# Performance work log

Measured on AMD Instinct MI355X. Metric: run time of the kernel, lower is better.

The kernel has to match this reference:

```python
import jax, jax.numpy as jnp
import numpy as np

# ---- model / data constants ----
B, N, D, L = 32, 96, 64, 5          # graphs, nodes per graph, hidden, layers
EP = 768                             # directed edges per graph (symmetrized in to_dense)
NODE_VOCAB = 11                      # matches LocalFWL2(..., 11, 5, 'instance')
EDGE_VOCAB = 5                       # edge labels 0..4; index 5 = 'no edge' embedding row
EPS = 1e-5


def setup_inputs() -> dict:
    key = jax.random.key(0)
    ks = jax.random.split(key, 12)
    # block-contiguous batch: graph b owns nodes [b*N, (b+1)*N)
    x = jax.random.randint(ks[0], (B * N,), 0, NODE_VOCAB)
    u = jax.random.randint(ks[1], (B, EP), 0, N)
    v = jax.random.randint(ks[2], (B, EP), 0, N)
    off = (jnp.arange(B) * N)[:, None]
    edge_index = jnp.stack([(u + off).reshape(-1), (v + off).reshape(-1)], axis=0)
    edge_attr = jax.random.randint(ks[3], (B * EP,), 0, EDGE_VOCAB)
    s = 0.1
    inv = 1.0 / np.sqrt(D)
    return {
        "x": x,
        "edge_index": edge_index,
        "edge_attr": edge_attr,
        "node_emb": jax.random.normal(ks[4], (NODE_VOCAB, D), jnp.float32) * s,
        "edge_emb": jax.random.normal(ks[5], (EDGE_VOCAB + 1, D), jnp.float32) * s,
        "W1": jax.random.normal(ks[6], (L, D, D), jnp.float32) * inv,
        "b1": jnp.zeros((L, D), jnp.float32),
        "W2": jax.random.normal(ks[7], (L, D, D), jnp.float32) * inv,
        "b2": jnp.zeros((L, D), jnp.float32),
        "Wm": jax.random.normal(ks[8], (L, D, D), jnp.float32) * inv,
        "bm": jnp.zeros((L, D), jnp.float32),
        "gamma": jnp.ones((L, D), jnp.float32),
        "beta": jnp.zeros((L, D), jnp.float32),
        "pool_w": jax.random.normal(ks[9], (D, 1), jnp.float32) * inv,
        "pool_b": jnp.zeros((1,), jnp.float32),
    }


def reference(x, edge_index, edge_attr, node_emb, edge_emb,
              W1, b1, W2, b2, Wm, bm, gamma, beta, pool_w, pool_b):
    # ---- to_dense: sparse edge list -> dense per-graph edge-label matrix ----
    g = edge_index[0] // N
    u = edge_index[0] % N
    v = edge_index[1] % N
    A = jnp.full((B, N, N), EDGE_VOCAB, dtype=jnp.int32)        # EDGE_VOCAB = no-edge
    ea = edge_attr.astype(jnp.int32)
    A = A.at[g, u, v].set(ea)
    A = A.at[g, v, u].set(ea)                                    # undirected
    adj = (A != EDGE_VOCAB).astype(node_emb.dtype)               # [B,N,N]

    # ---- pair-state init: W_uv = h_u + h_v + edge_emb(A_uv) ----
    H = node_emb[x.reshape(B, N)]                                # [B,N,D]
    W = H[:, :, None, :] + H[:, None, :, :] + edge_emb[A]        # [B,N,N,D]

    # ---- local FWL(2) layers ----
    for l in range(L):
        h1 = jax.nn.relu(jnp.einsum('buwd,de->buwe', W, W1[l]) + b1[l])
        h2 = jax.nn.relu(jnp.einsum('bwvd,de->bwve', W, W2[l]) + b2[l])
        # aggregate over w restricted to neighbors of v (local FWL2)
        M = jnp.einsum('buwd,bwv,bwvd->buvd', h1, adj, h2)       # [B,N,N,D]
        W = W + jnp.einsum('buvd,de->buve', M, Wm[l]) + bm[l]
        # instance norm over the pair dims (u,v), per graph, per channel
        mu = W.mean(axis=(1, 2), keepdims=True)
        var = W.var(axis=(1, 2), keepdims=True)
        W = gamma[l] * (W - mu) * jax.lax.rsqrt(var + EPS) + beta[l]
        W = jax.nn.relu(W)

    # ---- pooling: sum over all pairs, then Linear(D, 1), squeeze ----
    pooled = W.sum(axis=(1, 2))                                  # [B,D]
    return (pooled @ pool_w + pool_b).squeeze(-1)                # [B]
```

## Files before the change

### kernel.cpp

```cpp
#include <hip/hip_runtime.h>
#include <hip/hip_bf16.h>

#define B_ 32
#define N_ 96
#define D_ 64
#define L_ 5
#define BE_ 24576
#define NN_ 9216
#define BNN_ 294912
#define EPS_ 1e-5f
#define INV_NN (1.0f/9216.0f)

typedef unsigned short u16;
typedef unsigned int u32;
typedef __attribute__((ext_vector_type(8))) short bf16x8;
typedef __attribute__((ext_vector_type(4))) float f32x4;

__device__ __forceinline__ float bf2f(u16 r){ return __uint_as_float(((u32)r) << 16); }
__device__ __forceinline__ u32 f2bf(float f){
  u32 u = __float_as_uint(f);
  return (u + 0x7fffu + ((u >> 16) & 1u)) >> 16;
}
__device__ __forceinline__ u32 pack2(float lo, float hi){
  return f2bf(lo) | (f2bf(hi) << 16);
}

__global__ void k_scatter(const int* __restrict__ ei, const int* __restrict__ ea,
                          int* __restrict__ A)
{
  int e = blockIdx.x * 256 + threadIdx.x;
  if (e >= BE_) return;
  int a = ei[e], bnode = ei[BE_ + e];
  int g = a / N_;
  int u = a % N_;
  int v = bnode % N_;
  int lab = ea[e] & 7;
  int base = g * NN_;
  atomicMax(&A[base + u * N_ + v], ((e + 1) << 3) | lab);
  atomicMax(&A[base + v * N_ + u], ((BE_ + e + 1) << 3) | lab);
}

__launch_bounds__(256)
__global__ void k_winit(const int* __restrict__ x, const int* __restrict__ A,
                        const float* __restrict__ nemb, const float* __restrict__ eemb,
                        u16* __restrict__ W)
{
  int gid = blockIdx.x * 256 + threadIdx.x;
  int d = (gid & 15) * 4;
  int p = gid >> 4;
  int b = p / NN_;
  int rem = p % NN_;
  int u = rem / N_;
  int v = rem % N_;
  int xu = x[b * N_ + u], xv = x[b * N_ + v];
  int pk = A[p];
  int lab = pk ? (pk & 7) : 5;
  float4 nu = *(const float4*)(nemb + xu * 64 + d);
  float4 nv = *(const float4*)(nemb + xv * 64 + d);
  float4 ee = *(const float4*)(eemb + lab * 64 + d);
  uint2 o;
  o.x = pack2(nu.x + nv.x + ee.x, nu.y + nv.y + ee.y);
  o.y = pack2(nu.z + nv.z + ee.z, nu.w + nv.w + ee.w);
  ((uint2*)W)[gid] = o;
}

__global__ void k_prep(const float* __restrict__ W1, const float* __restrict__ W2,
                       const float* __restrict__ Wm, u16* __restrict__ WT)
{
  int idx = blockIdx.x * 256 + threadIdx.x;
  if (idx >= 15 * 4096) return;
  int l3 = idx >> 12;
  int r  = idx & 4095;
  int e = r >> 6, d = r & 63;
  int l = l3 / 3, which = l3 % 3;
  const float* s = which == 0 ? W1 : which == 1 ? W2 : Wm;
  WT[idx] = (u16)f2bf(s[l * 4096 + d * 64 + e]);
}

__launch_bounds__(256, 4)
__global__ void k_lin2(const u16* __restrict__ W, const u16* __restrict__ WT1,
                       const u16* __restrict__ WT2,
                       const float* __restrict__ b1l, const float* __restrict__ b2l,
                       const int* __restrict__ A,
                       const float* __restrict__ pst, const float* __restrict__ gml,
                       const float* __restrict__ btl, float* __restrict__ nsF,
                       int use_norm, u16* __restrict__ h1, u16* __restrict__ g2)
{
  __shared__ u16 Cs[64 * 264];
  __shared__ float nsS[128];
  const int tid = threadIdx.x;
  const int wave = tid >> 6, lane = tid & 63;
  const int lm = lane & 15, lg = lane >> 4;
  const int b = blockIdx.x / 36;
  const int qbase = (blockIdx.x % 36) * 256;

  if (use_norm) {
    if (tid < 128) {
      const float* p = pst + ((size_t)b * 144) * 128 + tid;
      float a0 = 0.f, a1 = 0.f, a2 = 0.f, a3 = 0.f;
      for (int i = 0; i < 144; i += 4) {
        a0 += p[(size_t)i * 128];
        a1 += p[(size_t)(i + 1) * 128];
        a2 += p[(size_t)(i + 2) * 128];
        a3 += p[(size_t)(i + 3) * 128];
      }
      nsS[tid] = (a0 + a1) + (a2 + a3);
    }
    __syncthreads();
  }

  float sc[2][8], sh[2][8];
  if (use_norm) {
    #pragma unroll
    for (int s = 0; s < 2; ++s) {
      int d0 = s * 32 + lg * 8;
      #pragma unroll
      for (int j = 0; j < 8; ++j) {
        int d = d0 + j;
        float S1 = nsS[d], S2 = nsS[64 + d];
        float mu = S1 * INV_NN;
        float var = fmaf(S2, INV_NN, -mu * mu);
        float s0 = gml[d] * rsqrtf(var + EPS_);
        sc[s][j] = s0;
        sh[s][j] = fmaf(-mu, s0, btl[d]);
      }
    }
    if ((blockIdx.x % 36) == 0 && tid < 64) {
      float S1 = nsS[tid], S2 = nsS[64 + tid];
      float mu = S1 * INV_NN;
      float var = fmaf(S2, INV_NN, -mu * mu);
      float s0 = gml[tid] * rsqrtf(var + EPS_);
      nsF[((size_t)b * 64 + tid) * 2]     = s0;
      nsF[((size_t)b * 64 + tid) * 2 + 1] = fmaf(-mu, s0, btl[tid]);
    }
  } else {
    #pragma unroll
    for (int s = 0; s < 2; ++s)
      #pragma unroll
      for (int j = 0; j < 8; ++j) { sc[s][j] = 1.f; sh[s][j] = 0.f; }
  }

  bf16x8 bF[4][2];
  int flags[4];
  #pragma unroll
  for (int qt = 0; qt < 4; ++qt) {
    int q = qbase + wave * 64 + qt * 16 + lm;
    const u16* wrow = W + ((size_t)b * NN_ + q) * 64;
    flags[qt] = A[b * NN_ + q];
    #pragma unroll
    for (int s = 0; s < 2; ++s) {
      bf16x8 raw = *(const bf16x8*)(wrow + s * 32 + lg * 8);
      if (use_norm) {
        bf16x8 bb;
        #pragma unroll
        for (int j = 0; j < 8; ++j) {
          float v = bf2f((u16)raw[j]);
          v = fmaxf(fmaf(v, sc[s][j], sh[s][j]), 0.f);
          bb[j] = (short)f2bf(v);
        }
        bF[qt][s] = bb;
      } else {
        bF[qt][s] = raw;
      }
    }
  }

  const f32x4 zf = {0.f, 0.f, 0.f, 0.f};

  {
    bf16x8 aF[4][2];
    #pragma unroll
    for (int et = 0; et < 4; ++et)
      #pragma unroll
      for (int s = 0; s < 2; ++s)
        aF[et][s] = *(const bf16x8*)(WT1 + (et * 16 + lm) * 64 + s * 32 + lg * 8);
    float4 bsv[4];
    #pragma unroll
    for (int et = 0; et < 4; ++et) bsv[et] = *(const float4*)(b1l + et * 16 + lg * 4);
    #pragma unroll
    for (int qt = 0; qt < 4; ++qt) {
      f32x4 acc[4] = {zf, zf, zf, zf};
      #pragma unroll
      for (int s = 0; s < 2; ++s)
        #pragma unroll
        for (int et = 0; et < 4; ++et)
          acc[et] = __builtin_amdgcn_mfma_f32_16x16x32_bf16(aF[et][s], bF[qt][s], acc[et], 0, 0, 0);
      int col = wave * 64 + qt * 16 + lm;
      #pragma unroll
      for (int et = 0; et < 4; ++et) {
        float bv[4] = {bsv[et].x, bsv[et].y, bsv[et].z, bsv[et].w};
        #pragma unroll
        for (int r = 0; r < 4; ++r)
          Cs[(et * 16 + lg * 4 + r) * 264 + col] = (u16)f2bf(fmaxf(acc[et][r] + bv[r], 0.f));
      }
    }
  }
  __syncthreads();
  {
    u16* ob = h1 + (size_t)b * 64 * NN_ + qbase;
    for (int i = tid; i < 2048; i += 256) {
      int e = i >> 5, qc = (i & 31) * 8;
      uint4 val = *(const uint4*)&Cs[e * 264 + qc];
      *(uint4*)(ob + (size_t)e * NN_ + qc) = val;
    }
  }
  __syncthreads();

  {
    bf16x8 aF[4][2];
    #pragma unroll
    for (int et = 0; et < 4; ++et)
      #pragma unroll
      for (int s = 0; s < 2; ++s)
        aF[et][s] = *(const bf16x8*)(WT2 + (et * 16 + lm) * 64 + s * 32 + lg * 8);
    float4 bsv[4];
    #pragma unroll
    for (int et = 0; et < 4; ++et) bsv[et] = *(const float4*)(b2l + et * 16 + lg * 4);
    #pragma unroll
    for (int qt = 0; qt < 4; ++qt) {
      f32x4 acc[4] = {zf, zf, zf, zf};
      #pragma unroll
      for (int s = 0; s < 2; ++s)
        #pragma unroll
        for (int et = 0; et < 4; ++et)
          acc[et] = __builtin_amdgcn_mfma_f32_16x16x32_bf16(aF[et][s], bF[qt][s], acc[et], 0, 0, 0);
      int col = wave * 64 + qt * 16 + lm;
      #pragma unroll
      for (int et = 0; et < 4; ++et) {
        float bv[4] = {bsv[et].x, bsv[et].y, bsv[et].z, bsv[et].w};
        #pragma unroll
        for (int r = 0; r < 4; ++r) {
          float v = fmaxf(acc[et][r] + bv[r], 0.f);
          if (!flags[qt]) v = 0.f;
          Cs[(et * 16 + lg * 4 + r) * 264 + col] = (u16)f2bf(v);
        }
      }
    }
  }
  __syncthreads();
  {
    u16* ob = g2 + (size_t)b * 64 * NN_ + qbase;
    for (int i = tid; i < 2048; i += 256) {
      int e = i >> 5, qc = (i & 31) * 8;
      uint4 val = *(const uint4*)&Cs[e * 264 + qc];
      *(uint4*)(ob + (size_t)e * NN_ + qc) = val;
    }
  }
}

__launch_bounds__(256, 4)
__global__ void k_einsum(const u16* __restrict__ h1, const u16* __restrict__ g2n,
                         u16* __restrict__ M)
{
  __shared__ u32 Bt[96 * 60];
  u16* Cst = (u16*)Bt;
  const int tid = threadIdx.x;
  const int wave = tid >> 6, lane = tid & 63;
  const int lm = lane & 15, lg = lane >> 4;
  const int bd = blockIdx.x;
  const u16* h1p = h1 + (size_t)bd * NN_;
  const u16* g2p = g2n + (size_t)bd * NN_;
  const int u0 = (wave & 1) * 48, v0 = (wave >> 1) * 48;

  #pragma unroll
  for (int it = 0; it < 9; ++it) {
    int p = it * 256 + tid;
    int wp = p / 48, vh = (p % 48) * 2;
    u32 a = *(const u32*)(g2p + (2 * wp) * 96 + vh);
    u32 c = *(const u32*)(g2p + (2 * wp + 1) * 96 + vh);
    Bt[vh * 60 + wp]       = (a & 0xffffu) | (c << 16);
    Bt[(vh + 1) * 60 + wp] = (a >> 16) | (c & 0xffff0000u);
  }

  bf16x8 aF[3][3];
  #pragma unroll
  for (int t = 0; t < 3; ++t)
    #pragma unroll
    for (int s = 0; s < 3; ++s)
      aF[t][s] = *(const bf16x8*)(h1p + (u0 + t * 16 + lm) * 96 + s * 32 + lg * 8);
  __syncthreads();

  const f32x4 zf = {0.f, 0.f, 0.f, 0.f};
  f32x4 acc[3][3];
  #pragma unroll
  for (int i = 0; i < 3; ++i)
    #pragma unroll
    for (int j = 0; j < 3; ++j) acc[i][j] = zf;

  #pragma unroll
  for (int s = 0; s < 3; ++s) {
    bf16x8 bb[3];
    #pragma unroll
    for (int vt = 0; vt < 3; ++vt)
      bb[vt] = *(const bf16x8*)&Bt[(v0 + vt * 16 + lm) * 60 + s * 16 + lg * 4];
    #pragma unroll
    for (int ut = 0; ut < 3; ++ut)
      #pragma unroll
      for (int vt = 0; vt < 3; ++vt)
        acc[ut][vt] = __builtin_amdgcn_mfma_f32_16x16x32_bf16(aF[ut][s], bb[vt], acc[ut][vt], 0, 0, 0);
  }
  __syncthreads();

  #pragma unroll
  for (int ut = 0; ut < 3; ++ut)
    #pragma unroll
    for (int vt = 0; vt < 3; ++vt)
      #pragma unroll
      for (int r = 0; r < 4; ++r)
        Cst[(u0 + ut * 16 + lg * 4 + r) * 104 + v0 + vt * 16 + lm] = (u16)f2bf(acc[ut][vt][r]);
  __syncthreads();
  u16* Mp = M + (size_t)bd * NN_;
  for (int i = tid; i < 1152; i += 256) {
    int u = i / 12, vc = (i % 12) * 8;
    uint4 val = *(const uint4*)&Cst[u * 104 + vc];
    *(uint4*)(Mp + u * 96 + vc) = val;
  }
}

__launch_bounds__(128)
__global__ void k_update(const u16* __restrict__ M, const u16* __restrict__ WmT,
                         const float* __restrict__ bml, u16* __restrict__ W,
                         const float* __restrict__ nsF, int use_norm,
                         float* __restrict__ pst)
{
  __shared__ u16 Mt[64 * 64];
  __shared__ float red[2][128];
  const int tid = threadIdx.x;
  const int wave = tid >> 6, lane = tid & 63;
  const int lm = lane & 15, lg = lane >> 4;
  const int b = blockIdx.x / 144;
  const int qi = blockIdx.x % 144;
  const int qblk = qi * 64;

  bf16x8 aF[4][2];
  #pragma unroll
  for (int et = 0; et < 4; ++et)
    #pragma unroll
    for (int s = 0; s < 2; ++s)
      aF[et][s] = *(const bf16x8*)(WmT + (et * 16 + lm) * 64 + s * 32 + lg * 8);

  uint2 wres[2][4];
  #pragma unroll
  for (int qtL = 0; qtL < 2; ++qtL) {
    int qg = qblk + (wave * 2 + qtL) * 16 + lm;
    const u16* Wp = W + ((size_t)b * NN_ + qg) * 64;
    #pragma unroll
    for (int et = 0; et < 4; ++et)
      wres[qtL][et] = *(const uint2*)(Wp + et * 16 + lg * 4);
  }

  float scn[4][4], shn[4][4];
  if (use_norm) {
    #pragma unroll
    for (int et = 0; et < 4; ++et) {
      int e0 = et * 16 + lg * 4;
      float4 t0 = *(const float4*)(nsF + ((size_t)b * 64 + e0) * 2);
      float4 t1 = *(const float4*)(nsF + ((size_t)b * 64 + e0) * 2 + 4);
      scn[et][0] = t0.x; shn[et][0] = t0.y; scn[et][1] = t0.z; shn[et][1] = t0.w;
      scn[et][2] = t1.x; shn[et][2] = t1.y; scn[et][3] = t1.z; shn[et][3] = t1.w;
    }
  } else {
    #pragma unroll
    for (int et = 0; et < 4; ++et)
      #pragma unroll
      for (int r = 0; r < 4; ++r) { scn[et][r] = 1.f; shn[et][r] = 0.f; }
  }

  {
    const int dpl = tid >> 1;
    const int qob = tid & 1;
    const u16* Mb = M + (size_t)(b * 64 + dpl) * NN_ + qblk;
    #pragma unroll
    for (int t = 0; t < 4; ++t) {
      int qo = qob + t * 2;
      uint4 v = *(const uint4*)(Mb + qo * 8);
      u32 ws[4] = {v.x, v.y, v.z, v.w};
      #pragma unroll
      for (int h = 0; h < 4; ++h) {
        int j0 = h * 2;
        int q0 = qo * 8 + j0;
        int slot0 = (dpl >> 3) ^ j0 ^ (qo & 7);
        int slot1 = (dpl >> 3) ^ (j0 + 1) ^ (qo & 7);
        Mt[q0 * 64 + slot0 * 8 + (dpl & 7)]       = (u16)(ws[h] & 0xffffu);
        Mt[(q0 + 1) * 64 + slot1 * 8 + (dpl & 7)] = (u16)(ws[h] >> 16);
      }
    }
  }
  __syncthreads();

  const f32x4 zf = {0.f, 0.f, 0.f, 0.f};
  f32x4 acc[2][4];
  #pragma unroll
  for (int i = 0; i < 2; ++i)
    #pragma unroll
    for (int j = 0; j < 4; ++j) acc[i][j] = zf;

  #pragma unroll
  for (int qtL = 0; qtL < 2; ++qtL) {
    int ql = (wave * 2 + qtL) * 16 + lm;
    bf16x8 bF[2];
    #pragma unroll
    for (int s = 0; s < 2; ++s) {
      int slot = (s * 4 + lg) ^ (ql & 7) ^ ((ql >> 3) & 7);
      bF[s] = *(const bf16x8*)&Mt[ql * 64 + slot * 8];
    }
    #pragma unroll
    for (int s = 0; s < 2; ++s)
      #pragma unroll
      for (int et = 0; et < 4; ++et)
        acc[qtL][et] = __builtin_amdgcn_mfma_f32_16x16x32_bf16(aF[et][s], bF[s], acc[qtL][et], 0, 0, 0);
  }

  float s1[4][4], s2[4][4];
  #pragma unroll
  for (int i = 0; i < 4; ++i)
    #pragma unroll
    for (int j = 0; j < 4; ++j) { s1[i][j] = 0.f; s2[i][j] = 0.f; }

  #pragma unroll
  for (int et = 0; et < 4; ++et) {
    int e0 = et * 16 + lg * 4;
    float4 bs = *(const float4*)(bml + e0);
    float bv[4] = {bs.x, bs.y, bs.z, bs.w};
    #pragma unroll
    for (int qtL = 0; qtL < 2; ++qtL) {
      int qg = qblk + (wave * 2 + qtL) * 16 + lm;
      u16* Wp = W + ((size_t)b * NN_ + qg) * 64 + e0;
      uint2 wo = wres[qtL][et];
      float wv[4] = {bf2f((u16)(wo.x & 0xffff)), bf2f((u16)(wo.x >> 16)),
                     bf2f((u16)(wo.y & 0xffff)), bf2f((u16)(wo.y >> 16))};
      float o[4];
      #pragma unroll
      for (int r = 0; r < 4; ++r) {
        float res = use_norm ? fmaxf(fmaf(wv[r], scn[et][r], shn[et][r]), 0.f) : wv[r];
        float val = acc[qtL][et][r] + bv[r] + res;
        o[r] = val;
        s1[et][r] += val;
        s2[et][r] = fmaf(val, val, s2[et][r]);
      }
      uint2 ov;
      ov.x = pack2(o[0], o[1]);
      ov.y = pack2(o[2], o[3]);
      *(uint2*)Wp = ov;
    }
  }

  #pragma unroll
  for (int et = 0; et < 4; ++et)
    #pragma unroll
    for (int r = 0; r < 4; ++r) {
      float a = s1[et][r], c = s2[et][r];
      a += __shfl_xor(a, 1, 64); a += __shfl_xor(a, 2, 64);
      a += __shfl_xor(a, 4, 64); a += __shfl_xor(a, 8, 64);
      c += __shfl_xor(c, 1, 64); c += __shfl_xor(c, 2, 64);
      c += __shfl_xor(c, 4, 64); c += __shfl_xor(c, 8, 64);
      if (lm == 0) {
        int e = et * 16 + lg * 4 + r;
        red[wave][e]      = a;
        red[wave][64 + e] = c;
      }
    }
  __syncthreads();
  if (tid < 128)
    pst[((size_t)b * 144 + qi) * 128 + tid] = red[0][tid] + red[1][tid];
}

__launch_bounds__(256)
__global__ void k_pool(const u16* __restrict__ W,
                       const float* __restrict__ pst,
                       const float* __restrict__ gml, const float* __restrict__ btl,
                       const float* __restrict__ pw, const float* __restrict__ pb,
                       float* __restrict__ out)
{
  __shared__ float nsS[128];
  const int b = blockIdx.x / 24;
  const int chunk = blockIdx.x % 24;
  const int tid = threadIdx.x;
  if (tid < 128) {
    const float* p = pst + ((size_t)b * 144) * 128 + tid;
    float a0 = 0.f, a1 = 0.f, a2 = 0.f, a3 = 0.f;
    for (int i = 0; i < 144; i += 4) {
      a0 += p[(size_t)i * 128];
      a1 += p[(size_t)(i + 1) * 128];
      a2 += p[(size_t)(i + 2) * 128];
      a3 += p[(size_t)(i + 3) * 128];
    }
    nsS[tid] = (a0 + a1) + (a2 + a3);
  }
  __syncthreads();
  const int e = tid & 63;
  float S1 = nsS[e], S2 = nsS[64 + e];
  float mu = S1 * INV_NN;
  float var = fmaf(S2, INV_NN, -mu * mu);
  float rsig = rsqrtf(var + EPS_);
  float scl = gml[e] * rsig;
  float shf = fmaf(-mu, scl, btl[e]);
  float pwv = pw[e];
  const u16* base = W + (size_t)b * NN_ * 64 + chunk * 24576;
  float s = 0.f;
  for (int k = 0; k < 96; k++) {
    float w = bf2f(base[k * 256 + tid]);
    s += fmaxf(fmaf(w, scl, shf), 0.f) * pwv;
  }
  for (int o = 32; o; o >>= 1) s += __shfl_down(s, o, 64);
  __shared__ float rs[4];
  if ((tid & 63) == 0) rs[tid >> 6] = s;
  __syncthreads();
  if (tid == 0) {
    float t = rs[0] + rs[1] + rs[2] + rs[3];
    if (chunk == 0) t += pb[0];
    atomicAdd(&out[b], t);
  }
}

extern "C" void kernel_launch(void* const* d_in, const int* in_sizes, int n_in,
                              void* d_out, int out_size, void* d_ws, size_t ws_size,
                              hipStream_t stream) {
  const int*   x    = (const int*)d_in[0];
  const int*   ei   = (const int*)d_in[1];
  const int*   ea   = (const int*)d_in[2];
  const float* nemb = (const float*)d_in[3];
  const float* eemb = (const float*)d_in[4];
  const float* W1   = (const float*)d_in[5];
  const float* b1   = (const float*)d_in[6];
  const float* W2   = (const float*)d_in[7];
  const float* b2   = (const float*)d_in[8];
  const float* Wm   = (const float*)d_in[9];
  const float* bm   = (const float*)d_in[10];
  const float* gm   = (const float*)d_in[11];
  const float* bt   = (const float*)d_in[12];
  const float* pw   = (const float*)d_in[13];
  const float* pb   = (const float*)d_in[14];

  char* ws = (char*)d_ws;
  const size_t OFF_A  = 0;
  const size_t OFF_W  = 1179648;
  const size_t OFF_H1 = 38928384;
  const size_t OFF_G2 = 76677120;
  const size_t OFF_M  = 114425856;
  const size_t OFF_PS = 152174592;
  const size_t OFF_NF = 154533888;
  const size_t OFF_WT = 154550272;
  const size_t NEED   = OFF_WT + 122880;
  if (ws_size < NEED) return;

  int*   A     = (int*)(ws + OFF_A);
  u16*   W     = (u16*)(ws + OFF_W);
  u16*   h1    = (u16*)(ws + OFF_H1);
  u16*   g2n   = (u16*)(ws + OFF_G2);
  u16*   M     = (u16*)(ws + OFF_M);
  float* pst   = (float*)(ws + OFF_PS);
  float* nsF   = (float*)(ws + OFF_NF);
  u16*   WT    = (u16*)(ws + OFF_WT);
  float* out   = (float*)d_out;

  hipMemsetAsync(A, 0, 1179648, stream);
  hipMemsetAsync(out, 0, 32 * sizeof(float), stream);

  k_prep<<<240, 256, 0, stream>>>(W1, W2, Wm, WT);
  k_scatter<<<96, 256, 0, stream>>>(ei, ea, A);
  k_winit<<<18432, 256, 0, stream>>>(x, A, nemb, eemb, W);

  for (int l = 0; l < L_; l++) {
    int un = (l > 0);
    const float* gml = un ? gm + (l - 1) * 64 : gm;
    const float* btl = un ? bt + (l - 1) * 64 : bt;
    k_lin2<<<1152, 256, 0, stream>>>(W, WT + (l * 3 + 0) * 4096, WT + (l * 3 + 1) * 4096,
                                     b1 + l * 64, b2 + l * 64, A, pst, gml, btl, nsF,
                                     un, h1, g2n);
    k_einsum<<<2048, 256, 0, stream>>>(h1, g2n, M);
    k_update<<<4608, 128, 0, stream>>>(M, WT + (l * 3 + 2) * 4096, bm + l * 64, W,
                                       nsF, un, pst);
  }
  k_pool<<<768, 256, 0, stream>>>(W, pst, gm + 4 * 64, bt + 4 * 64, pw, pb, out);
}
```

Baseline: 551.0 us.

## Hoist instance-norm stats into separate kernel and halve k_lin2 tile

Moves the per-graph instance-norm reduction (summing 144 partial stat rows) out of every k_lin2 and k_pool block into a small k_ns kernel that writes scale/shift once per graph. k_lin2 then just loads precomputed scale/shift. Its tile is halved to 128 pairs per block with smaller shared memory, doubling the grid and raising the occupancy hint to 8. This removes redundant reduction work done by every block, at the cost of extra kernel launches per layer.

```diff
diff --git a/kernel.cpp b/kernel.cpp
--- a/kernel.cpp
+++ b/kernel.cpp
@@ -77,37 +77,46 @@
   WT[idx] = (u16)f2bf(s[l * 4096 + d * 64 + e]);
 }
 
-__launch_bounds__(256, 4)
+__launch_bounds__(128)
+__global__ void k_ns(const float* __restrict__ pst, const float* __restrict__ gml,
+                     const float* __restrict__ btl, float* __restrict__ nsF)
+{
+  __shared__ float nsS[128];
+  const int b = blockIdx.x;
+  const int tid = threadIdx.x;
+  const float* p = pst + ((size_t)b * 144) * 128 + tid;
+  float a0 = 0.f, a1 = 0.f, a2 = 0.f, a3 = 0.f;
+  for (int i = 0; i < 144; i += 4) {
+    a0 += p[(size_t)i * 128];
+    a1 += p[(size_t)(i + 1) * 128];
+    a2 += p[(size_t)(i + 2) * 128];
+    a3 += p[(size_t)(i + 3) * 128];
+  }
+  nsS[tid] = (a0 + a1) + (a2 + a3);
+  __syncthreads();
+  if (tid < 64) {
+    float S1 = nsS[tid], S2 = nsS[64 + tid];
+    float mu = S1 * INV_NN;
+    float var = fmaf(S2, INV_NN, -mu * mu);
+    float s0 = gml[tid] * rsqrtf(var + EPS_);
+    nsF[((size_t)b * 64 + tid) * 2]     = s0;
+    nsF[((size_t)b * 64 + tid) * 2 + 1] = fmaf(-mu, s0, btl[tid]);
+  }
+}
+
+__launch_bounds__(256, 8)
 __global__ void k_lin2(const u16* __restrict__ W, const u16* __restrict__ WT1,
                        const u16* __restrict__ WT2,
                        const float* __restrict__ b1l, const float* __restrict__ b2l,
-                       const int* __restrict__ A,
-                       const float* __restrict__ pst, const float* __restrict__ gml,
-                       const float* __restrict__ btl, float* __restrict__ nsF,
+                       const int* __restrict__ A, const float* __restrict__ nsF,
                        int use_norm, u16* __restrict__ h1, u16* __restrict__ g2)
 {
-  __shared__ u16 Cs[64 * 264];
-  __shared__ float nsS[128];
+  __shared__ u16 Cs[64 * 136];
   const int tid = threadIdx.x;
   const int wave = tid >> 6, lane = tid & 63;
   const int lm = lane & 15, lg = lane >> 4;
-  const int b = blockIdx.x / 36;
-  const int qbase = (blockIdx.x % 36) * 256;
-
-  if (use_norm) {
-    if (tid < 128) {
-      const float* p = pst + ((size_t)b * 144) * 128 + tid;
-      float a0 = 0.f, a1 = 0.f, a2 = 0.f, a3 = 0.f;
-      for (int i = 0; i < 144; i += 4) {
-        a0 += p[(size_t)i * 128];
-        a1 += p[(size_t)(i + 1) * 128];
-        a2 += p[(size_t)(i + 2) * 128];
-        a3 += p[(size_t)(i + 3) * 128];
-      }
-      nsS[tid] = (a0 + a1) + (a2 + a3);
-    }
-    __syncthreads();
-  }
+  const int b = blockIdx.x / 72;
+  const int qbase = (blockIdx.x % 72) * 128;
 
   float sc[2][8], sh[2][8];
   if (use_norm) {
@@ -115,23 +124,10 @@
     for (int s = 0; s < 2; ++s) {
       int d0 = s * 32 + lg * 8;
       #pragma unroll
-      for (int j = 0; j < 8; ++j) {
-        int d = d0 + j;
-        float S1 = nsS[d], S2 = nsS[64 + d];
-        float mu = S1 * INV_NN;
-        float var = fmaf(S2, INV_NN, -mu * mu);
-        float s0 = gml[d] * rsqrtf(var + EPS_);
-        sc[s][j] = s0;
-        sh[s][j] = fmaf(-mu, s0, btl[d]);
-      }
-    }
-    if ((blockIdx.x % 36) == 0 && tid < 64) {
-      float S1 = nsS[tid], S2 = nsS[64 + tid];
-      float mu = S1 * INV_NN;
-      float var = fmaf(S2, INV_NN, -mu * mu);
-      float s0 = gml[tid] * rsqrtf(var + EPS_);
-      nsF[((size_t)b * 64 + tid) * 2]     = s0;
-      nsF[((size_t)b * 64 + tid) * 2 + 1] = fmaf(-mu, s0, btl[tid]);
+      for (int j = 0; j < 8; j += 2) {
+        float4 t = *(const float4*)(nsF + ((size_t)b * 64 + d0 + j) * 2);
+        sc[s][j] = t.x; sh[s][j] = t.y; sc[s][j + 1] = t.z; sh[s][j + 1] = t.w;
+      }
     }
   } else {
     #pragma unroll
@@ -140,11 +136,11 @@
       for (int j = 0; j < 8; ++j) { sc[s][j] = 1.f; sh[s][j] = 0.f; }
   }
 
-  bf16x8 bF[4][2];
-  int flags[4];
-  #pragma unroll
-  for (int qt = 0; qt < 4; ++qt) {
-    int q = qbase + wave * 64 + qt * 16 + lm;
+  bf16x8 bF[2][2];
+  int flags[2];
+  #pragma unroll
+  for (int qt = 0; qt < 2; ++qt) {
+    int q = qbase + wave * 32 + qt * 16 + lm;
     const u16* wrow = W + ((size_t)b * NN_ + q) * 64;
     flags[qt] = A[b * NN_ + q];
     #pragma unroll
@@ -178,29 +174,29 @@
     #pragma unroll
     for (int et = 0; et < 4; ++et) bsv[et] = *(const float4*)(b1l + et * 16 + lg * 4);
     #pragma unroll
-    for (int qt = 0; qt < 4; ++qt) {
+    for (int qt = 0; qt < 2; ++qt) {
       f32x4 acc[4] = {zf, zf, zf, zf};
       #pragma unroll
       for (int s = 0; s < 2; ++s)
         #pragma unroll
         for (int et = 0; et < 4; ++et)
           acc[et] = __builtin_amdgcn_mfma_f32_16x16x32_bf16(aF[et][s], bF[qt][s], acc[et], 0, 0, 0);
-      int col = wave * 64 + qt * 16 + lm;
+      int col = wave * 32 + qt * 16 + lm;
       #pragma unroll
       for (int et = 0; et < 4; ++et) {
         float bv[4] = {bsv[et].x, bsv[et].y, bsv[et].z, bsv[et].w};
         #pragma unroll
         for (int r = 0; r < 4; ++r)
-          Cs[(et * 16 + lg * 4 + r) * 264 + col] = (u16)f2bf(fmaxf(acc[et][r] + bv[r], 0.f));
+          Cs[(et * 16 + lg * 4 + r) * 136 + col] = (u16)f2bf(fmaxf(acc[et][r] + bv[r], 0.f));
       }
     }
   }
   __syncthreads();
   {
     u16* ob = h1 + (size_t)b * 64 * NN_ + qbase;
-    for (int i = tid; i < 2048; i += 256) {
-      int e = i >> 5, qc = (i & 31) * 8;
-      uint4 val = *(const uint4*)&Cs[e * 264 + qc];
+    for (int i = tid; i < 1024; i += 256) {
+      int e = i >> 4, qc = (i & 15) * 8;
+      uint4 val = *(const uint4*)&Cs[e * 136 + qc];
       *(uint4*)(ob + (size_t)e * NN_ + qc) = val;
     }
   }
@@ -217,14 +213,14 @@
     #pragma unroll
     for (int et = 0; et < 4; ++et) bsv[et] = *(const float4*)(b2l + et * 16 + lg * 4);
     #pragma unroll
-    for (int qt = 0; qt < 4; ++qt) {
+    for (int qt = 0; qt < 2; ++qt) {
       f32x4 acc[4] = {zf, zf, zf, zf};
       #pragma unroll
       for (int s = 0; s < 2; ++s)
         #pragma unroll
         for (int et = 0; et < 4; ++et)
           acc[et] = __builtin_amdgcn_mfma_f32_16x16x32_bf16(aF[et][s], bF[qt][s], acc[et], 0, 0, 0);
-      int col = wave * 64 + qt * 16 + lm;
+      int col = wave * 32 + qt * 16 + lm;
       #pragma unroll
       for (int et = 0; et < 4; ++et) {
         float bv[4] = {bsv[et].x, bsv[et].y, bsv[et].z, bsv[et].w};
@@ -232,7 +228,7 @@
         for (int r = 0; r < 4; ++r) {
           float v = fmaxf(acc[et][r] + bv[r], 0.f);
           if (!flags[qt]) v = 0.f;
-          Cs[(et * 16 + lg * 4 + r) * 264 + col] = (u16)f2bf(v);
+          Cs[(et * 16 + lg * 4 + r) * 136 + col] = (u16)f2bf(v);
         }
       }
     }
@@ -240,9 +236,9 @@
   __syncthreads();
   {
     u16* ob = g2 + (size_t)b * 64 * NN_ + qbase;
-    for (int i = tid; i < 2048; i += 256) {
-      int e = i >> 5, qc = (i & 31) * 8;
-      uint4 val = *(const uint4*)&Cs[e * 264 + qc];
+    for (int i = tid; i < 1024; i += 256) {
+      int e = i >> 4, qc = (i & 15) * 8;
+      uint4 val = *(const uint4*)&Cs[e * 136 + qc];
       *(uint4*)(ob + (size_t)e * NN_ + qc) = val;
     }
   }
@@ -467,34 +463,16 @@
 
 __launch_bounds__(256)
 __global__ void k_pool(const u16* __restrict__ W,
-                       const float* __restrict__ pst,
-                       const float* __restrict__ gml, const float* __restrict__ btl,
+                       const float* __restrict__ nsF,
                        const float* __restrict__ pw, const float* __restrict__ pb,
                        float* __restrict__ out)
 {
-  __shared__ float nsS[128];
   const int b = blockIdx.x / 24;
   const int chunk = blockIdx.x % 24;
   const int tid = threadIdx.x;
-  if (tid < 128) {
-    const float* p = pst + ((size_t)b * 144) * 128 + tid;
-    float a0 = 0.f, a1 = 0.f, a2 = 0.f, a3 = 0.f;
-    for (int i = 0; i < 144; i += 4) {
-      a0 += p[(size_t)i * 128];
-      a1 += p[(size_t)(i + 1) * 128];
-      a2 += p[(size_t)(i + 2) * 128];
-      a3 += p[(size_t)(i + 3) * 128];
-    }
-    nsS[tid] = (a0 + a1) + (a2 + a3);
-  }
-  __syncthreads();
   const int e = tid & 63;
-  float S1 = nsS[e], S2 = nsS[64 + e];
-  float mu = S1 * INV_NN;
-  float var = fmaf(S2, INV_NN, -mu * mu);
-  float rsig = rsqrtf(var + EPS_);
-  float scl = gml[e] * rsig;
-  float shf = fmaf(-mu, scl, btl[e]);
+  float scl = nsF[((size_t)b * 64 + e) * 2];
+  float shf = nsF[((size_t)b * 64 + e) * 2 + 1];
   float pwv = pw[e];
   const u16* base = W + (size_t)b * NN_ * 64 + chunk * 24576;
   float s = 0.f;
@@ -563,14 +541,14 @@
 
   for (int l = 0; l < L_; l++) {
     int un = (l > 0);
-    const float* gml = un ? gm + (l - 1) * 64 : gm;
-    const float* btl = un ? bt + (l - 1) * 64 : bt;
-    k_lin2<<<1152, 256, 0, stream>>>(W, WT + (l * 3 + 0) * 4096, WT + (l * 3 + 1) * 4096,
-                                     b1 + l * 64, b2 + l * 64, A, pst, gml, btl, nsF,
-                                     un, h1, g2n);
+    if (un)
+      k_ns<<<32, 128, 0, stream>>>(pst, gm + (l - 1) * 64, bt + (l - 1) * 64, nsF);
+    k_lin2<<<2304, 256, 0, stream>>>(W, WT + (l * 3 + 0) * 4096, WT + (l * 3 + 1) * 4096,
+                                     b1 + l * 64, b2 + l * 64, A, nsF, un, h1, g2n);
     k_einsum<<<2048, 256, 0, stream>>>(h1, g2n, M);
     k_update<<<4608, 128, 0, stream>>>(M, WT + (l * 3 + 2) * 4096, bm + l * 64, W,
                                        nsF, un, pst);
   }
-  k_pool<<<768, 256, 0, stream>>>(W, pst, gm + 4 * 64, bt + 4 * 64, pw, pb, out);
-}
+  k_ns<<<32, 128, 0, stream>>>(pst, gm + 4 * 64, bt + 4 * 64, nsF);
+  k_pool<<<768, 256, 0, stream>>>(W, nsF, pw, pb, out);
+}
```

Result: slower. 633.4 us (+14.9%).
